# Kernel tuning notes

Measured on AMD Instinct MI355X. Metric: run time of the kernel, lower is better.

Reference implementation:

```python
import jax, jax.numpy as jnp
import numpy as np

EPS = 1e-6
HEAD_DIM = 64
N_Q = 16
N_KV = 2

def setup_inputs() -> dict:
    key = jax.random.key(0)
    ks = jax.random.split(key, 4)
    H = 1024
    x = jax.random.normal(ks[0], (4, 8192, H), dtype=jnp.float32)
    ln_weight = jnp.zeros((H,), dtype=jnp.float32)  # Gemma param; scale is (1 + w)
    wq = jax.random.normal(ks[1], (H, HEAD_DIM * N_Q), dtype=jnp.float32) / np.sqrt(H)
    wk = jax.random.normal(ks[2], (H, HEAD_DIM * N_KV), dtype=jnp.float32) / np.sqrt(H)
    wv = jax.random.normal(ks[3], (H, HEAD_DIM * N_KV), dtype=jnp.float32) / np.sqrt(H)
    return {"x": x, "ln_weight": ln_weight, "wq": wq, "wk": wk, "wv": wv}

def gemma_rms_norm(x, w):
    xf = x.astype(jnp.float32)
    h = xf * jax.lax.rsqrt(jnp.mean(xf * xf, axis=-1, keepdims=True) + EPS)
    return (h * (1.0 + w.astype(jnp.float32))).astype(x.dtype)

def reference(x, ln_weight, wq, wk, wv):
    # Gemma RMSNorm prologue, then three linear projections (no bias).
    h = gemma_rms_norm(x, ln_weight)            # [B, S, H]
    q = jnp.einsum('bsh,hd->bsd', h, wq)        # [B, S, nq*d]
    k = jnp.einsum('bsh,hd->bsd', h, wk)        # [B, S, nkv*d]
    v = jnp.einsum('bsh,hd->bsd', h, wv)
    B, S = x.shape[0], x.shape[1]
    q = q.reshape(B, S, N_Q, HEAD_DIM)
    k = k.reshape(B, S, N_KV, HEAD_DIM)
    v = v.reshape(B, S, N_KV, HEAD_DIM)
    return (q, k, v)
```

## Files before the change

### kernel.cpp

```cpp
#include <hip/hip_runtime.h>
#include <hip/hip_bf16.h>

typedef __attribute__((ext_vector_type(4))) float f32x4;
typedef __attribute__((ext_vector_type(8))) short bf16x8;

#define H 1024
#define NTOT 1280
#define BM 128
#define BN 128
#define BK 64
#define NKT 16
#define NTILES 10

static __device__ __forceinline__ unsigned short f2bf(float f) {
    __hip_bfloat16 b = __float2bfloat16(f);
    return __builtin_bit_cast(unsigned short, b);
}

#define GLOAD_LDS16(g, l)                                                     \
    __builtin_amdgcn_global_load_lds(                                         \
        (const __attribute__((address_space(1))) void*)(g),                   \
        (__attribute__((address_space(3))) void*)(l), 16, 0, 0)

__global__ __launch_bounds__(256) void k_rms(const float* __restrict__ x,
                                             __hip_bfloat16* __restrict__ h) {
    const int wave = threadIdx.x >> 6;
    const int lane = threadIdx.x & 63;
    const size_t row = (size_t)blockIdx.x * 4 + wave;

    const float4* xr = (const float4*)(x + row * H);
    float4 v[4];
    float ss = 0.f;
#pragma unroll
    for (int i = 0; i < 4; ++i) {
        v[i] = xr[lane + 64 * i];
        ss += v[i].x * v[i].x + v[i].y * v[i].y + v[i].z * v[i].z + v[i].w * v[i].w;
    }
#pragma unroll
    for (int o = 1; o < 64; o <<= 1) ss += __shfl_xor(ss, o);
    const float sc = rsqrtf(ss * (1.0f / H) + 1e-6f);

    ushort4* hr = (ushort4*)(h + row * H);
#pragma unroll
    for (int i = 0; i < 4; ++i) {
        ushort4 o4;
        o4.x = f2bf(v[i].x * sc);
        o4.y = f2bf(v[i].y * sc);
        o4.z = f2bf(v[i].z * sc);
        o4.w = f2bf(v[i].w * sc);
        hr[lane + 64 * i] = o4;
    }
}

__global__ __launch_bounds__(256) void k_wprep(const float* __restrict__ wq,
                                               const float* __restrict__ wk,
                                               const float* __restrict__ wv,
                                               const float* __restrict__ lnw,
                                               __hip_bfloat16* __restrict__ Bt) {
    __shared__ float l[64][65];
    const int t = threadIdx.x;
    const int kt = blockIdx.x & 15;
    const int ntl = blockIdx.x >> 4;
    const int k0 = kt * 64, n0 = ntl * 64;
    const float* src; int ldn, nb;
    if (n0 < 1024)      { src = wq; ldn = 1024; nb = n0; }
    else if (n0 < 1152) { src = wk; ldn = 128;  nb = n0 - 1024; }
    else                { src = wv; ldn = 128;  nb = n0 - 1152; }
    const int nl = t & 63, kl = t >> 6;
#pragma unroll
    for (int i = 0; i < 16; ++i) {
        const int k = kl + i * 4;
        l[k][nl] = (1.0f + lnw[k0 + k]) * src[(size_t)(k0 + k) * ldn + nb + nl];
    }
    __syncthreads();
    const int k2 = t & 63, n2 = t >> 6;
#pragma unroll
    for (int i = 0; i < 16; ++i) {
        const int n = n2 + i * 4;
        Bt[(size_t)(n0 + n) * 1024 + k0 + k2] = __float2bfloat16(l[k2][n]);
    }
}

__global__ __launch_bounds__(256, 2) void k_gemm(const __hip_bfloat16* __restrict__ A,
                                                 const __hip_bfloat16* __restrict__ Bt,
                                                 float* __restrict__ out, int rows) {
    __shared__ __align__(16) char smem[65536];

    const int tid = threadIdx.x;
    const int lane = tid & 63;
    const int wid = tid >> 6;
    const int wm = wid >> 1;
    const int wn = wid & 1;

    const int cpx = gridDim.x >> 3;
    const int wg = (blockIdx.x & 7) * cpx + (blockIdx.x >> 3);
    const int nt = wg % NTILES;
    const int mt = wg / NTILES;
    const size_t m0 = (size_t)mt * BM;

    const int r = tid >> 3;
    const int cswz = ((tid & 7) * 16) ^ ((r & 7) << 4);
    const char* aG = (const char*)A + (m0 + r) * (size_t)(H * 2) + cswz;
    const char* bG = (const char*)Bt + ((size_t)nt * BN + r) * (size_t)(H * 2) + cswz;

#define STAGE(buf, kt)                                                        \
    {                                                                         \
        _Pragma("unroll") for (int q = 0; q < 4; ++q)                         \
            GLOAD_LDS16(aG + (size_t)(kt) * 128 + (size_t)q * 32 * (H * 2),   \
                        smem + (buf) * 32768 + q * 4096 + tid * 16);          \
        _Pragma("unroll") for (int q = 0; q < 4; ++q)                         \
            GLOAD_LDS16(bG + (size_t)(kt) * 128 + (size_t)q * 32 * (H * 2),   \
                        smem + (buf) * 32768 + 16384 + q * 4096 + tid * 16);  \
    }

    const int rowA = wm * 64 + (lane & 15);
    const int rowB = wn * 64 + (lane & 15);
    const int xm = (lane & 7) << 4;
    const int c0 = (((lane >> 4) * 16)) ^ xm;
    const int c1 = (64 + ((lane >> 4) * 16)) ^ xm;

    f32x4 acc[4][4] = {};

#define TILE(cur, kt, DS, VM)                                                 \
    {                                                                         \
        const char* aL = smem + (cur) * 32768;                                \
        const char* bL = aL + 16384;                                          \
        asm volatile("s_waitcnt vmcnt(" VM ")" ::: "memory");                 \
        __builtin_amdgcn_s_barrier();                                         \
        bf16x8 a0[4], b0[4];                                                  \
        _Pragma("unroll") for (int mi = 0; mi < 4; ++mi)                      \
            a0[mi] = *(const bf16x8*)(aL + (rowA + mi * 16) * 128 + c0);      \
        _Pragma("unroll") for (int ni = 0; ni < 4; ++ni)                      \
            b0[ni] = *(const bf16x8*)(bL + (rowB + ni * 16) * 128 + c0);      \
        __builtin_amdgcn_s_setprio(1);                                        \
        _Pragma("unroll") for (int mi = 0; mi < 4; ++mi)                      \
            _Pragma("unroll") for (int ni = 0; ni < 4; ++ni)                  \
                acc[mi][ni] = __builtin_amdgcn_mfma_f32_16x16x32_bf16(        \
                    a0[mi], b0[ni], acc[mi][ni], 0, 0, 0);                    \
        __builtin_amdgcn_s_setprio(0);                                        \
        bf16x8 a1[4], b1[4];                                                  \
        _Pragma("unroll") for (int mi = 0; mi < 4; ++mi)                      \
            a1[mi] = *(const bf16x8*)(aL + (rowA + mi * 16) * 128 + c1);      \
        _Pragma("unroll") for (int ni = 0; ni < 4; ++ni)                      \
            b1[ni] = *(const bf16x8*)(bL + (rowB + ni * 16) * 128 + c1);      \
        asm volatile("s_waitcnt lgkmcnt(0)" ::: "memory");                    \
        __builtin_amdgcn_sched_barrier(0);                                    \
        __builtin_amdgcn_s_barrier();                                         \
        __builtin_amdgcn_sched_barrier(0);                                    \
        if (DS) STAGE(cur, (kt) + 2);                                         \
        __builtin_amdgcn_s_setprio(1);                                        \
        _Pragma("unroll") for (int mi = 0; mi < 4; ++mi)                      \
            _Pragma("unroll") for (int ni = 0; ni < 4; ++ni)                  \
                acc[mi][ni] = __builtin_amdgcn_mfma_f32_16x16x32_bf16(        \
                    a1[mi], b1[ni], acc[mi][ni], 0, 0, 0);                    \
        __builtin_amdgcn_s_setprio(0);                                        \
    }

    STAGE(0, 0);
    STAGE(1, 1);

    for (int kt = 0; kt < NKT - 4; kt += 2) {
        TILE(0, kt, 1, "8");
        TILE(1, kt + 1, 1, "8");
    }
    TILE(0, NKT - 4, 1, "8");
    TILE(1, NKT - 3, 1, "8");
    TILE(0, NKT - 2, 0, "8");
    TILE(1, NKT - 1, 0, "0");

    const size_t QSZ = (size_t)rows * 1024;
    const size_t KSZ = (size_t)rows * 128;
    const int colg0 = nt * BN + wn * 64;
    float* op;
    int ldc, cb0;
    if (colg0 < 1024)      { op = out;             ldc = 1024; cb0 = colg0; }
    else if (colg0 < 1152) { op = out + QSZ;       ldc = 128;  cb0 = colg0 - 1024; }
    else                   { op = out + QSZ + KSZ; ldc = 128;  cb0 = colg0 - 1152; }

    const size_t r0 = m0 + wm * 64 + ((lane >> 4) * 4);
    const int cc0 = cb0 + (lane & 15);
#pragma unroll
    for (int mi = 0; mi < 4; ++mi)
#pragma unroll
        for (int ni = 0; ni < 4; ++ni)
#pragma unroll
            for (int rr = 0; rr < 4; ++rr)
                op[(r0 + mi * 16 + rr) * (size_t)ldc + cc0 + ni * 16] = acc[mi][ni][rr];
}

extern "C" void kernel_launch(void* const* d_in, const int* in_sizes, int n_in,
                              void* d_out, int out_size, void* d_ws, size_t ws_size,
                              hipStream_t stream) {
    const float* x   = (const float*)d_in[0];
    const float* lnw = (const float*)d_in[1];
    const float* wq  = (const float*)d_in[2];
    const float* wk  = (const float*)d_in[3];
    const float* wv  = (const float*)d_in[4];
    float* out = (float*)d_out;

    const int rows = in_sizes[0] / H;

    __hip_bfloat16* Bt = (__hip_bfloat16*)d_ws;
    __hip_bfloat16* h  = (__hip_bfloat16*)((char*)d_ws + (size_t)NTOT * H * 2);

    k_wprep<<<320, 256, 0, stream>>>(wq, wk, wv, lnw, Bt);
    k_rms<<<rows / 4, 256, 0, stream>>>(x, h);
    k_gemm<<<(rows / BM) * NTILES, 256, 0, stream>>>(h, Bt, out, rows);
}
```

Measured before the change: 142.6 us.

## Prepack weights in MFMA fragment order and load B straight to registers

The weight prep kernel now writes B in a fragment-major layout that matches the MFMA 16x16x32 operand order. The GEMM then loads B fragments directly from global memory into registers, double-buffered one k-tile ahead, and no longer stages B through LDS. LDS use is halved to 32KB, which lets the launch bound rise to 3 blocks per CU. In exchange, each wave fetches its own B fragments from global/L2 with no sharing between the wm waves, and register pressure goes up.

```diff
diff --git a/kernel.cpp b/kernel.cpp
--- a/kernel.cpp
+++ b/kernel.cpp
@@ -56,7 +56,7 @@
                                                const float* __restrict__ wk,
                                                const float* __restrict__ wv,
                                                const float* __restrict__ lnw,
-                                               __hip_bfloat16* __restrict__ Bt) {
+                                               __hip_bfloat16* __restrict__ Bf) {
     __shared__ float l[64][65];
     const int t = threadIdx.x;
     const int kt = blockIdx.x & 15;
@@ -73,18 +73,25 @@
         l[k][nl] = (1.0f + lnw[k0 + k]) * src[(size_t)(k0 + k) * ldn + nb + nl];
     }
     __syncthreads();
-    const int k2 = t & 63, n2 = t >> 6;
-#pragma unroll
-    for (int i = 0; i < 16; ++i) {
-        const int n = n2 + i * 4;
-        Bt[(size_t)(n0 + n) * 1024 + k0 + k2] = __float2bfloat16(l[k2][n]);
-    }
-}
-
-__global__ __launch_bounds__(256, 2) void k_gemm(const __hip_bfloat16* __restrict__ A,
-                                                 const __hip_bfloat16* __restrict__ Bt,
+#pragma unroll
+    for (int s2 = 0; s2 < 2; ++s2) {
+        const int s = t + s2 * 256;
+        const int fi = s >> 6, lane = s & 63;
+        const int n16l = fi & 3, k32l = fi >> 2;
+        const int col = lane & 15, kq = lane >> 4;
+        bf16x8 pk;
+#pragma unroll
+        for (int j = 0; j < 8; ++j)
+            pk[j] = f2bf(l[k32l * 32 + kq * 8 + j][n16l * 16 + col]);
+        const size_t fr = (size_t)(ntl * 4 + n16l) * 32 + (kt * 2 + k32l);
+        *(bf16x8*)((char*)Bf + (fr << 10) + lane * 16) = pk;
+    }
+}
+
+__global__ __launch_bounds__(256, 3) void k_gemm(const __hip_bfloat16* __restrict__ A,
+                                                 const __hip_bfloat16* __restrict__ Bf,
                                                  float* __restrict__ out, int rows) {
-    __shared__ __align__(16) char smem[65536];
+    __shared__ __align__(16) char smem[32768];
 
     const int tid = threadIdx.x;
     const int lane = tid & 63;
@@ -101,72 +108,80 @@
     const int r = tid >> 3;
     const int cswz = ((tid & 7) * 16) ^ ((r & 7) << 4);
     const char* aG = (const char*)A + (m0 + r) * (size_t)(H * 2) + cswz;
-    const char* bG = (const char*)Bt + ((size_t)nt * BN + r) * (size_t)(H * 2) + cswz;
-
-#define STAGE(buf, kt)                                                        \
-    {                                                                         \
-        _Pragma("unroll") for (int q = 0; q < 4; ++q)                         \
-            GLOAD_LDS16(aG + (size_t)(kt) * 128 + (size_t)q * 32 * (H * 2),   \
-                        smem + (buf) * 32768 + q * 4096 + tid * 16);          \
-        _Pragma("unroll") for (int q = 0; q < 4; ++q)                         \
-            GLOAD_LDS16(bG + (size_t)(kt) * 128 + (size_t)q * 32 * (H * 2),   \
-                        smem + (buf) * 32768 + 16384 + q * 4096 + tid * 16);  \
-    }
+
+#define STAGE_A(buf, kt)                                                      \
+    _Pragma("unroll") for (int q = 0; q < 4; ++q)                             \
+        GLOAD_LDS16(aG + (size_t)(kt) * 128 + (size_t)q * 32 * (H * 2),       \
+                    smem + (buf) * 16384 + q * 4096 + tid * 16);
+
+    const int n16b = nt * 8 + wn * 4;
+    const char* bF = (const char*)Bf + lane * 16;
+
+#define BLOAD(dst, kt)                                                        \
+    _Pragma("unroll") for (int ni = 0; ni < 4; ++ni)                          \
+        _Pragma("unroll") for (int kk = 0; kk < 2; ++kk)                      \
+            dst[ni * 2 + kk] = *(const bf16x8*)(bF +                          \
+                (((size_t)(n16b + ni) * 32 + (size_t)(kt) * 2 + kk) << 10));
 
     const int rowA = wm * 64 + (lane & 15);
-    const int rowB = wn * 64 + (lane & 15);
     const int xm = (lane & 7) << 4;
     const int c0 = (((lane >> 4) * 16)) ^ xm;
     const int c1 = (64 + ((lane >> 4) * 16)) ^ xm;
 
     f32x4 acc[4][4] = {};
-
-#define TILE(cur, kt, DS, VM)                                                 \
+    bf16x8 bA[8], bB[8];
+
+#define TILE(cur, kt, BN_, DS_, bcur, bnext, VM)                              \
     {                                                                         \
-        const char* aL = smem + (cur) * 32768;                                \
-        const char* bL = aL + 16384;                                          \
+        const char* aL = smem + (cur) * 16384;                                \
         asm volatile("s_waitcnt vmcnt(" VM ")" ::: "memory");                 \
+        __builtin_amdgcn_sched_barrier(0);                                    \
         __builtin_amdgcn_s_barrier();                                         \
-        bf16x8 a0[4], b0[4];                                                  \
+        __builtin_amdgcn_sched_barrier(0);                                    \
+        bf16x8 a0[4];                                                         \
         _Pragma("unroll") for (int mi = 0; mi < 4; ++mi)                      \
             a0[mi] = *(const bf16x8*)(aL + (rowA + mi * 16) * 128 + c0);      \
-        _Pragma("unroll") for (int ni = 0; ni < 4; ++ni)                      \
-            b0[ni] = *(const bf16x8*)(bL + (rowB + ni * 16) * 128 + c0);      \
+        if (BN_) BLOAD(bnext, (kt) + 1);                                      \
+        asm volatile("s_waitcnt lgkmcnt(0)" ::: "memory");                    \
+        __builtin_amdgcn_sched_barrier(0);                                    \
         __builtin_amdgcn_s_setprio(1);                                        \
         _Pragma("unroll") for (int mi = 0; mi < 4; ++mi)                      \
             _Pragma("unroll") for (int ni = 0; ni < 4; ++ni)                  \
                 acc[mi][ni] = __builtin_amdgcn_mfma_f32_16x16x32_bf16(        \
-                    a0[mi], b0[ni], acc[mi][ni], 0, 0, 0);                    \
+                    a0[mi], bcur[ni * 2 + 0], acc[mi][ni], 0, 0, 0);          \
         __builtin_amdgcn_s_setprio(0);                                        \
-        bf16x8 a1[4], b1[4];                                                  \
+        bf16x8 a1[4];                                                         \
         _Pragma("unroll") for (int mi = 0; mi < 4; ++mi)                      \
             a1[mi] = *(const bf16x8*)(aL + (rowA + mi * 16) * 128 + c1);      \
-        _Pragma("unroll") for (int ni = 0; ni < 4; ++ni)                      \
-            b1[ni] = *(const bf16x8*)(bL + (rowB + ni * 16) * 128 + c1);      \
         asm volatile("s_waitcnt lgkmcnt(0)" ::: "memory");                    \
         __builtin_amdgcn_sched_barrier(0);                                    \
         __builtin_amdgcn_s_barrier();                                         \
         __builtin_amdgcn_sched_barrier(0);                                    \
-        if (DS) STAGE(cur, (kt) + 2);                                         \
+        if (DS_) STAGE_A(cur, (kt) + 2);                                      \
         __builtin_amdgcn_s_setprio(1);                                        \
         _Pragma("unroll") for (int mi = 0; mi < 4; ++mi)                      \
             _Pragma("unroll") for (int ni = 0; ni < 4; ++ni)                  \
                 acc[mi][ni] = __builtin_amdgcn_mfma_f32_16x16x32_bf16(        \
-                    a1[mi], b1[ni], acc[mi][ni], 0, 0, 0);                    \
+                    a1[mi], bcur[ni * 2 + 1], acc[mi][ni], 0, 0, 0);          \
         __builtin_amdgcn_s_setprio(0);                                        \
     }
 
-    STAGE(0, 0);
-    STAGE(1, 1);
-
-    for (int kt = 0; kt < NKT - 4; kt += 2) {
-        TILE(0, kt, 1, "8");
-        TILE(1, kt + 1, 1, "8");
-    }
-    TILE(0, NKT - 4, 1, "8");
-    TILE(1, NKT - 3, 1, "8");
-    TILE(0, NKT - 2, 0, "8");
-    TILE(1, NKT - 1, 0, "0");
+    STAGE_A(0, 0);
+    STAGE_A(1, 1);
+    BLOAD(bA, 0);
+    asm volatile("s_waitcnt vmcnt(0)" ::: "memory");
+    __builtin_amdgcn_sched_barrier(0);
+    __builtin_amdgcn_s_barrier();
+    __builtin_amdgcn_sched_barrier(0);
+
+    for (int kt = 0; kt < 12; kt += 2) {
+        TILE(0, kt, 1, 1, bA, bB, "4");
+        TILE(1, kt + 1, 1, 1, bB, bA, "4");
+    }
+    TILE(0, 12, 1, 1, bA, bB, "4");
+    TILE(1, 13, 1, 1, bB, bA, "4");
+    TILE(0, 14, 1, 0, bA, bB, "4");
+    TILE(1, 15, 0, 0, bB, bA, "0");
 
     const size_t QSZ = (size_t)rows * 1024;
     const size_t KSZ = (size_t)rows * 128;
@@ -200,10 +215,10 @@
 
     const int rows = in_sizes[0] / H;
 
-    __hip_bfloat16* Bt = (__hip_bfloat16*)d_ws;
+    __hip_bfloat16* Bf = (__hip_bfloat16*)d_ws;
     __hip_bfloat16* h  = (__hip_bfloat16*)((char*)d_ws + (size_t)NTOT * H * 2);
 
-    k_wprep<<<320, 256, 0, stream>>>(wq, wk, wv, lnw, Bt);
+    k_wprep<<<320, 256, 0, stream>>>(wq, wk, wv, lnw, Bf);
     k_rms<<<rows / 4, 256, 0, stream>>>(x, h);
-    k_gemm<<<(rows / BM) * NTILES, 256, 0, stream>>>(h, Bt, out, rows);
-}
+    k_gemm<<<(rows / BM) * NTILES, 256, 0, stream>>>(h, Bf, out, rows);
+}
```

Result: slower. 150.6 us (+5.6%).

## Fuse RMSNorm into GEMM by loading fp32 x and scaling rows in epilogue

Applied to the files above, without the earlier changes.

Removes the separate RMS normalization kernel and its bf16 intermediate buffer. The GEMM now loads fp32 x through registers, converts it to bf16 into LDS, accumulates per-row sums of squares on the fly, and applies the rsqrt scale to the accumulators in the epilogue. This avoids writing and re-reading the normalized activation. In exchange, the fp32 input is re-read by every N-tile block, and A staging now goes through registers instead of direct-to-LDS loads, which raises register pressure and changes the pipeline synchronization.

```diff
diff --git a/kernel.cpp b/kernel.cpp
--- a/kernel.cpp
+++ b/kernel.cpp
@@ -21,36 +21,6 @@
     __builtin_amdgcn_global_load_lds(                                         \
         (const __attribute__((address_space(1))) void*)(g),                   \
         (__attribute__((address_space(3))) void*)(l), 16, 0, 0)
-
-__global__ __launch_bounds__(256) void k_rms(const float* __restrict__ x,
-                                             __hip_bfloat16* __restrict__ h) {
-    const int wave = threadIdx.x >> 6;
-    const int lane = threadIdx.x & 63;
-    const size_t row = (size_t)blockIdx.x * 4 + wave;
-
-    const float4* xr = (const float4*)(x + row * H);
-    float4 v[4];
-    float ss = 0.f;
-#pragma unroll
-    for (int i = 0; i < 4; ++i) {
-        v[i] = xr[lane + 64 * i];
-        ss += v[i].x * v[i].x + v[i].y * v[i].y + v[i].z * v[i].z + v[i].w * v[i].w;
-    }
-#pragma unroll
-    for (int o = 1; o < 64; o <<= 1) ss += __shfl_xor(ss, o);
-    const float sc = rsqrtf(ss * (1.0f / H) + 1e-6f);
-
-    ushort4* hr = (ushort4*)(h + row * H);
-#pragma unroll
-    for (int i = 0; i < 4; ++i) {
-        ushort4 o4;
-        o4.x = f2bf(v[i].x * sc);
-        o4.y = f2bf(v[i].y * sc);
-        o4.z = f2bf(v[i].z * sc);
-        o4.w = f2bf(v[i].w * sc);
-        hr[lane + 64 * i] = o4;
-    }
-}
 
 __global__ __launch_bounds__(256) void k_wprep(const float* __restrict__ wq,
                                                const float* __restrict__ wk,
@@ -81,10 +51,11 @@
     }
 }
 
-__global__ __launch_bounds__(256, 2) void k_gemm(const __hip_bfloat16* __restrict__ A,
+__global__ __launch_bounds__(256, 2) void k_gemm(const float* __restrict__ X,
                                                  const __hip_bfloat16* __restrict__ Bt,
                                                  float* __restrict__ out, int rows) {
     __shared__ __align__(16) char smem[65536];
+    __shared__ float s_lds[BM];
 
     const int tid = threadIdx.x;
     const int lane = tid & 63;
@@ -98,20 +69,38 @@
     const int mt = wg / NTILES;
     const size_t m0 = (size_t)mt * BM;
 
-    const int r = tid >> 3;
-    const int cswz = ((tid & 7) * 16) ^ ((r & 7) << 4);
-    const char* aG = (const char*)A + (m0 + r) * (size_t)(H * 2) + cswz;
-    const char* bG = (const char*)Bt + ((size_t)nt * BN + r) * (size_t)(H * 2) + cswz;
-
-#define STAGE(buf, kt)                                                        \
-    {                                                                         \
-        _Pragma("unroll") for (int q = 0; q < 4; ++q)                         \
-            GLOAD_LDS16(aG + (size_t)(kt) * 128 + (size_t)q * 32 * (H * 2),   \
-                        smem + (buf) * 32768 + q * 4096 + tid * 16);          \
-        _Pragma("unroll") for (int q = 0; q < 4; ++q)                         \
-            GLOAD_LDS16(bG + (size_t)(kt) * 128 + (size_t)q * 32 * (H * 2),   \
-                        smem + (buf) * 32768 + 16384 + q * 4096 + tid * 16);  \
-    }
+    const int rA = tid >> 3;
+    const float* xb = X + (m0 + rA) * (size_t)H + (tid & 7) * 8;
+    const int awz = ((tid & 7) * 16) ^ ((rA & 7) << 4);
+
+    const char* bG = (const char*)Bt + ((size_t)nt * BN + rA) * (size_t)(H * 2)
+                     + (((tid & 7) * 16) ^ ((rA & 7) << 4));
+
+    float4 va[8];
+    float ssq[4] = {0.f, 0.f, 0.f, 0.f};
+
+#define A_ISSUE(kt)                                                           \
+    _Pragma("unroll") for (int q = 0; q < 4; ++q) {                           \
+        va[q * 2]     = *(const float4*)(xb + (size_t)q * 32 * H + (kt) * 64);\
+        va[q * 2 + 1] = *(const float4*)(xb + (size_t)q * 32 * H + (kt) * 64 + 4); \
+    }
+
+#define A_CVT(buf)                                                            \
+    _Pragma("unroll") for (int q = 0; q < 4; ++q) {                           \
+        float4 f0 = va[q * 2], f1 = va[q * 2 + 1];                            \
+        ssq[q] += f0.x * f0.x + f0.y * f0.y + f0.z * f0.z + f0.w * f0.w;      \
+        ssq[q] += f1.x * f1.x + f1.y * f1.y + f1.z * f1.z + f1.w * f1.w;      \
+        bf16x8 pk;                                                            \
+        pk[0] = f2bf(f0.x); pk[1] = f2bf(f0.y); pk[2] = f2bf(f0.z);           \
+        pk[3] = f2bf(f0.w); pk[4] = f2bf(f1.x); pk[5] = f2bf(f1.y);           \
+        pk[6] = f2bf(f1.z); pk[7] = f2bf(f1.w);                               \
+        *(bf16x8*)(smem + (buf) * 32768 + rA * 128 + q * 4096 + awz) = pk;    \
+    }
+
+#define STAGE_B(buf, kt)                                                      \
+    _Pragma("unroll") for (int q = 0; q < 4; ++q)                             \
+        GLOAD_LDS16(bG + (size_t)(kt) * 128 + (size_t)q * 32 * (H * 2),       \
+                    smem + (buf) * 32768 + 16384 + q * 4096 + tid * 16);
 
     const int rowA = wm * 64 + (lane & 15);
     const int rowB = wn * 64 + (lane & 15);
@@ -121,17 +110,17 @@
 
     f32x4 acc[4][4] = {};
 
-#define TILE(cur, kt, DS, VM)                                                 \
+#define TILE(cur, kt, DS, TAIL)                                               \
     {                                                                         \
         const char* aL = smem + (cur) * 32768;                                \
         const char* bL = aL + 16384;                                          \
-        asm volatile("s_waitcnt vmcnt(" VM ")" ::: "memory");                 \
-        __builtin_amdgcn_s_barrier();                                         \
+        if (DS) A_ISSUE((kt) + 2);                                            \
         bf16x8 a0[4], b0[4];                                                  \
         _Pragma("unroll") for (int mi = 0; mi < 4; ++mi)                      \
             a0[mi] = *(const bf16x8*)(aL + (rowA + mi * 16) * 128 + c0);      \
         _Pragma("unroll") for (int ni = 0; ni < 4; ++ni)                      \
             b0[ni] = *(const bf16x8*)(bL + (rowB + ni * 16) * 128 + c0);      \
+        asm volatile("s_waitcnt lgkmcnt(0)" ::: "memory");                    \
         __builtin_amdgcn_s_setprio(1);                                        \
         _Pragma("unroll") for (int mi = 0; mi < 4; ++mi)                      \
             _Pragma("unroll") for (int ni = 0; ni < 4; ++ni)                  \
@@ -144,29 +133,55 @@
         _Pragma("unroll") for (int ni = 0; ni < 4; ++ni)                      \
             b1[ni] = *(const bf16x8*)(bL + (rowB + ni * 16) * 128 + c1);      \
         asm volatile("s_waitcnt lgkmcnt(0)" ::: "memory");                    \
+        __builtin_amdgcn_s_barrier();          \
         __builtin_amdgcn_sched_barrier(0);                                    \
-        __builtin_amdgcn_s_barrier();                                         \
-        __builtin_amdgcn_sched_barrier(0);                                    \
-        if (DS) STAGE(cur, (kt) + 2);                                         \
+        if (DS) {                                                             \
+            STAGE_B(cur, (kt) + 2);                                           \
+            asm volatile("s_waitcnt vmcnt(4)" ::: "memory");                  \
+            A_CVT(cur);                                                       \
+        }                                                                     \
+        if (TAIL) asm volatile("s_waitcnt vmcnt(0)" ::: "memory");            \
         __builtin_amdgcn_s_setprio(1);                                        \
         _Pragma("unroll") for (int mi = 0; mi < 4; ++mi)                      \
             _Pragma("unroll") for (int ni = 0; ni < 4; ++ni)                  \
                 acc[mi][ni] = __builtin_amdgcn_mfma_f32_16x16x32_bf16(        \
                     a1[mi], b1[ni], acc[mi][ni], 0, 0, 0);                    \
         __builtin_amdgcn_s_setprio(0);                                        \
-    }
-
-    STAGE(0, 0);
-    STAGE(1, 1);
-
-    for (int kt = 0; kt < NKT - 4; kt += 2) {
-        TILE(0, kt, 1, "8");
-        TILE(1, kt + 1, 1, "8");
-    }
-    TILE(0, NKT - 4, 1, "8");
-    TILE(1, NKT - 3, 1, "8");
-    TILE(0, NKT - 2, 0, "8");
-    TILE(1, NKT - 1, 0, "0");
+        asm volatile("s_waitcnt lgkmcnt(0)" ::: "memory");                    \
+        __builtin_amdgcn_sched_barrier(0);                                    \
+        __builtin_amdgcn_s_barrier();                                         \
+        __builtin_amdgcn_sched_barrier(0);                                    \
+    }
+
+    A_ISSUE(0);
+    STAGE_B(0, 0);
+    asm volatile("s_waitcnt vmcnt(4)" ::: "memory");
+    A_CVT(0);
+    A_ISSUE(1);
+    STAGE_B(1, 1);
+    asm volatile("s_waitcnt vmcnt(4)" ::: "memory");
+    A_CVT(1);
+    asm volatile("s_waitcnt lgkmcnt(0)" ::: "memory");
+    __builtin_amdgcn_sched_barrier(0);
+    __builtin_amdgcn_s_barrier();
+    __builtin_amdgcn_sched_barrier(0);
+
+    for (int kt = 0; kt < 14; kt += 2) {
+        TILE(0, kt, 1, 0);
+        TILE(1, kt + 1, 1, 0);
+    }
+    TILE(0, 14, 0, 1);
+    TILE(1, 15, 0, 0);
+
+#pragma unroll
+    for (int q = 0; q < 4; ++q) {
+        float s = ssq[q];
+        s += __shfl_xor(s, 1);
+        s += __shfl_xor(s, 2);
+        s += __shfl_xor(s, 4);
+        if ((tid & 7) == 0) s_lds[rA + q * 32] = rsqrtf(s * (1.0f / H) + 1e-6f);
+    }
+    __syncthreads();
 
     const size_t QSZ = (size_t)rows * 1024;
     const size_t KSZ = (size_t)rows * 128;
@@ -177,15 +192,19 @@
     else if (colg0 < 1152) { op = out + QSZ;       ldc = 128;  cb0 = colg0 - 1024; }
     else                   { op = out + QSZ + KSZ; ldc = 128;  cb0 = colg0 - 1152; }
 
-    const size_t r0 = m0 + wm * 64 + ((lane >> 4) * 4);
+    const int rl0 = wm * 64 + ((lane >> 4) * 4);
+    const size_t r0 = m0 + rl0;
     const int cc0 = cb0 + (lane & 15);
 #pragma unroll
     for (int mi = 0; mi < 4; ++mi)
 #pragma unroll
-        for (int ni = 0; ni < 4; ++ni)
-#pragma unroll
-            for (int rr = 0; rr < 4; ++rr)
-                op[(r0 + mi * 16 + rr) * (size_t)ldc + cc0 + ni * 16] = acc[mi][ni][rr];
+        for (int rr = 0; rr < 4; ++rr) {
+            const float sc = s_lds[rl0 + mi * 16 + rr];
+#pragma unroll
+            for (int ni = 0; ni < 4; ++ni)
+                op[(r0 + mi * 16 + rr) * (size_t)ldc + cc0 + ni * 16] =
+                    acc[mi][ni][rr] * sc;
+        }
 }
 
 extern "C" void kernel_launch(void* const* d_in, const int* in_sizes, int n_in,
@@ -201,9 +220,7 @@
     const int rows = in_sizes[0] / H;
 
     __hip_bfloat16* Bt = (__hip_bfloat16*)d_ws;
-    __hip_bfloat16* h  = (__hip_bfloat16*)((char*)d_ws + (size_t)NTOT * H * 2);
 
     k_wprep<<<320, 256, 0, stream>>>(wq, wk, wv, lnw, Bt);
-    k_rms<<<rows / 4, 256, 0, stream>>>(x, h);
-    k_gemm<<<(rows / BM) * NTILES, 256, 0, stream>>>(h, Bt, out, rows);
-}
+    k_gemm<<<(rows / BM) * NTILES, 256, 0, stream>>>(x, Bt, out, rows);
+}
```

Result: slower. 192.6 us (+35.1%).

## Widen GEMM tile to 128x256 with BK=32 and 1x4 wave layout

Applied to the files above, without the earlier changes.

Changes the GEMM block tile from 128x128 to 128x256 with a K-step of 32. Each wave now covers all 128 rows and 64 columns, so it holds an 8x4 grid of accumulators. The LDS staging uses a new pair-row swizzled layout over 48KB of double-buffered shared memory. The aim is to raise arithmetic intensity per block, cut redundant A-tile loads across N tiles, and reduce the LDS footprint. The cost is twice as many pipeline iterations with more barriers, more accumulator registers, and fewer blocks in the grid.

```diff
diff --git a/kernel.cpp b/kernel.cpp
--- a/kernel.cpp
+++ b/kernel.cpp
@@ -7,10 +7,10 @@
 #define H 1024
 #define NTOT 1280
 #define BM 128
-#define BN 128
-#define BK 64
-#define NKT 16
-#define NTILES 10
+#define BN 256
+#define BK 32
+#define NKT2 32
+#define NTILES 5
 
 static __device__ __forceinline__ unsigned short f2bf(float f) {
     __hip_bfloat16 b = __float2bfloat16(f);
@@ -84,13 +84,11 @@
 __global__ __launch_bounds__(256, 2) void k_gemm(const __hip_bfloat16* __restrict__ A,
                                                  const __hip_bfloat16* __restrict__ Bt,
                                                  float* __restrict__ out, int rows) {
-    __shared__ __align__(16) char smem[65536];
+    __shared__ __align__(16) char smem[49152];
 
     const int tid = threadIdx.x;
     const int lane = tid & 63;
-    const int wid = tid >> 6;
-    const int wm = wid >> 1;
-    const int wn = wid & 1;
+    const int wn = tid >> 6;
 
     const int cpx = gridDim.x >> 3;
     const int wg = (blockIdx.x & 7) * cpx + (blockIdx.x >> 3);
@@ -98,75 +96,81 @@
     const int mt = wg / NTILES;
     const size_t m0 = (size_t)mt * BM;
 
-    const int r = tid >> 3;
-    const int cswz = ((tid & 7) * 16) ^ ((r & 7) << 4);
-    const char* aG = (const char*)A + (m0 + r) * (size_t)(H * 2) + cswz;
-    const char* bG = (const char*)Bt + ((size_t)nt * BN + r) * (size_t)(H * 2) + cswz;
+    const char* aSrc[2];
+#pragma unroll
+    for (int j = 0; j < 2; ++j) {
+        const int d = tid + j * 256;
+        const int rp = d >> 3, s = (d & 7) ^ (rp & 7);
+        aSrc[j] = (const char*)A + (m0 + rp * 2 + (s >> 2)) * (size_t)(H * 2)
+                  + (s & 3) * 16;
+    }
+    const char* bSrc[4];
+#pragma unroll
+    for (int j = 0; j < 4; ++j) {
+        const int d = tid + j * 256;
+        const int rp = d >> 3, s = (d & 7) ^ (rp & 7);
+        bSrc[j] = (const char*)Bt + ((size_t)nt * BN + rp * 2 + (s >> 2)) * (size_t)(H * 2)
+                  + (s & 3) * 16;
+    }
 
 #define STAGE(buf, kt)                                                        \
     {                                                                         \
-        _Pragma("unroll") for (int q = 0; q < 4; ++q)                         \
-            GLOAD_LDS16(aG + (size_t)(kt) * 128 + (size_t)q * 32 * (H * 2),   \
-                        smem + (buf) * 32768 + q * 4096 + tid * 16);          \
-        _Pragma("unroll") for (int q = 0; q < 4; ++q)                         \
-            GLOAD_LDS16(bG + (size_t)(kt) * 128 + (size_t)q * 32 * (H * 2),   \
-                        smem + (buf) * 32768 + 16384 + q * 4096 + tid * 16);  \
-    }
-
-    const int rowA = wm * 64 + (lane & 15);
-    const int rowB = wn * 64 + (lane & 15);
-    const int xm = (lane & 7) << 4;
-    const int c0 = (((lane >> 4) * 16)) ^ xm;
-    const int c1 = (64 + ((lane >> 4) * 16)) ^ xm;
-
-    f32x4 acc[4][4] = {};
+        _Pragma("unroll") for (int j = 0; j < 2; ++j)                         \
+            GLOAD_LDS16(aSrc[j] + (size_t)(kt) * 64,                          \
+                        smem + (buf) * 24576 + (tid + j * 256) * 16);         \
+        _Pragma("unroll") for (int j = 0; j < 4; ++j)                         \
+            GLOAD_LDS16(bSrc[j] + (size_t)(kt) * 64,                          \
+                        smem + (buf) * 24576 + 8192 + (tid + j * 256) * 16);  \
+    }
+
+    const int fb = ((lane & 15) >> 1) * 128
+                 + (((((lane & 1) << 2) + (lane >> 4)) ^ ((lane & 15) >> 1)) << 4);
+    const int bb = wn * 4096 + fb;
+
+    f32x4 acc[8][4] = {};
 
 #define TILE(cur, kt, DS, VM)                                                 \
     {                                                                         \
-        const char* aL = smem + (cur) * 32768;                                \
-        const char* bL = aL + 16384;                                          \
+        const char* aL = smem + (cur) * 24576;                                \
+        const char* bL = aL + 8192;                                           \
         asm volatile("s_waitcnt vmcnt(" VM ")" ::: "memory");                 \
         __builtin_amdgcn_s_barrier();                                         \
-        bf16x8 a0[4], b0[4];                                                  \
-        _Pragma("unroll") for (int mi = 0; mi < 4; ++mi)                      \
-            a0[mi] = *(const bf16x8*)(aL + (rowA + mi * 16) * 128 + c0);      \
+        bf16x8 af[4], bf_[4];                                                 \
+        _Pragma("unroll") for (int mi = 0; mi < 4; ++mi)                      \
+            af[mi] = *(const bf16x8*)(aL + fb + mi * 1024);                   \
         _Pragma("unroll") for (int ni = 0; ni < 4; ++ni)                      \
-            b0[ni] = *(const bf16x8*)(bL + (rowB + ni * 16) * 128 + c0);      \
+            bf_[ni] = *(const bf16x8*)(bL + bb + ni * 1024);                  \
+        asm volatile("s_waitcnt lgkmcnt(0)" ::: "memory");                    \
         __builtin_amdgcn_s_setprio(1);                                        \
         _Pragma("unroll") for (int mi = 0; mi < 4; ++mi)                      \
             _Pragma("unroll") for (int ni = 0; ni < 4; ++ni)                  \
                 acc[mi][ni] = __builtin_amdgcn_mfma_f32_16x16x32_bf16(        \
-                    a0[mi], b0[ni], acc[mi][ni], 0, 0, 0);                    \
+                    af[mi], bf_[ni], acc[mi][ni], 0, 0, 0);                   \
         __builtin_amdgcn_s_setprio(0);                                        \
-        bf16x8 a1[4], b1[4];                                                  \
-        _Pragma("unroll") for (int mi = 0; mi < 4; ++mi)                      \
-            a1[mi] = *(const bf16x8*)(aL + (rowA + mi * 16) * 128 + c1);      \
-        _Pragma("unroll") for (int ni = 0; ni < 4; ++ni)                      \
-            b1[ni] = *(const bf16x8*)(bL + (rowB + ni * 16) * 128 + c1);      \
+        bf16x8 ag[4];                                                         \
+        _Pragma("unroll") for (int mi = 0; mi < 4; ++mi)                      \
+            ag[mi] = *(const bf16x8*)(aL + fb + (mi + 4) * 1024);             \
         asm volatile("s_waitcnt lgkmcnt(0)" ::: "memory");                    \
-        __builtin_amdgcn_sched_barrier(0);                                    \
-        __builtin_amdgcn_s_barrier();                                         \
+        __builtin_amdgcn_s_barrier();              \
         __builtin_amdgcn_sched_barrier(0);                                    \
         if (DS) STAGE(cur, (kt) + 2);                                         \
         __builtin_amdgcn_s_setprio(1);                                        \
         _Pragma("unroll") for (int mi = 0; mi < 4; ++mi)                      \
             _Pragma("unroll") for (int ni = 0; ni < 4; ++ni)                  \
-                acc[mi][ni] = __builtin_amdgcn_mfma_f32_16x16x32_bf16(        \
-                    a1[mi], b1[ni], acc[mi][ni], 0, 0, 0);                    \
+                acc[mi + 4][ni] = __builtin_amdgcn_mfma_f32_16x16x32_bf16(    \
+                    ag[mi], bf_[ni], acc[mi + 4][ni], 0, 0, 0);               \
         __builtin_amdgcn_s_setprio(0);                                        \
     }
 
     STAGE(0, 0);
     STAGE(1, 1);
 
-    for (int kt = 0; kt < NKT - 4; kt += 2) {
-        TILE(0, kt, 1, "8");
-        TILE(1, kt + 1, 1, "8");
-    }
-    TILE(0, NKT - 4, 1, "8");
-    TILE(1, NKT - 3, 1, "8");
-    TILE(0, NKT - 2, 0, "8");
-    TILE(1, NKT - 1, 0, "0");
+    for (int kt = 0; kt < NKT2 - 2; kt += 2) {
+        TILE(0, kt, 1, "6");
+        TILE(1, kt + 1, 1, "6");
+    }
+    TILE(0, NKT2 - 2, 0, "6");
+    TILE(1, NKT2 - 1, 0, "0");
 
     const size_t QSZ = (size_t)rows * 1024;
     const size_t KSZ = (size_t)rows * 128;
@@ -177,10 +181,10 @@
     else if (colg0 < 1152) { op = out + QSZ;       ldc = 128;  cb0 = colg0 - 1024; }
     else                   { op = out + QSZ + KSZ; ldc = 128;  cb0 = colg0 - 1152; }
 
-    const size_t r0 = m0 + wm * 64 + ((lane >> 4) * 4);
+    const size_t r0 = m0 + ((lane >> 4) * 4);
     const int cc0 = cb0 + (lane & 15);
 #pragma unroll
-    for (int mi = 0; mi < 4; ++mi)
+    for (int mi = 0; mi < 8; ++mi)
 #pragma unroll
         for (int ni = 0; ni < 4; ++ni)
 #pragma unroll
```

New measurement: 144.4 us. No clear change (+1.2%).
